# Kernel optimization log

Hardware: AMD Instinct MI355X
Metric: run time of the kernel (lower is better)

## Reference

```python
import jax, jax.numpy as jnp
import numpy as np

N, ND, NPAIR, KS = 131072, 32, 6, 3  # batch, dijetFeatures, 6 dijets, kernel=stride=3

def setup_inputs() -> dict:
    key = jax.random.key(0)
    k1, k2, k3, k4 = jax.random.split(key, 4)
    x = jax.random.normal(k1, (N, ND, 2 * NPAIR), dtype=jnp.float32)
    d = jax.random.normal(k2, (N, ND, NPAIR), dtype=jnp.float32)
    # Conv1d(nd, nd, 3, stride=3) params, torch layout [out_ch, in_ch, k]
    fan_in = ND * KS
    W = jax.random.normal(k3, (ND, ND, KS), dtype=jnp.float32) / np.float32(np.sqrt(fan_in))
    b = jax.random.normal(k4, (ND,), dtype=jnp.float32) * 0.01
    return {"x": x, "d": d, "W": W, "b": b}

def reference(x, d, W, b):
    n = x.shape[0]
    # reinforce interleave: (j0 j1 d0 | j2 j3 d1 | ...) -> [n, nd, 6, 3]
    # x[:, :, 2s:2s+2] followed by d[:, :, s] for each of the 6 slots.
    din = jnp.concatenate([x.reshape(n, ND, NPAIR, 2), d[..., None]], axis=3)
    # Conv1d kernel=stride=3 over the length-18 interleaved seq == per-slot contraction
    out = jnp.einsum('ncsk,ock->nos', din, W) + b[None, :, None]
    return out  # [n, nd, 6]
```

## Files before the change

### kernel.cpp

```cpp
#include <hip/hip_runtime.h>


#define ND 32
#define NPAIR 6
#define SPB 32
#define BT 192
#define COLS (SPB * NPAIR)
#define KSTR 104
#define OSTR 200

typedef __attribute__((ext_vector_type(8))) short bf16x8;
typedef __attribute__((ext_vector_type(4))) float f32x4;

__device__ __forceinline__ unsigned pack2(float lo, float hi) {
    return __builtin_amdgcn_perm(__float_as_uint(hi), __float_as_uint(lo), 0x07060302u);
}
__device__ __forceinline__ unsigned short bf16t(float v) {
    return (unsigned short)(__float_as_uint(v) >> 16);
}

__global__ __launch_bounds__(BT) void dijet_mfma(
    const float* __restrict__ x,
    const float* __restrict__ d,
    const float* __restrict__ W,
    const float* __restrict__ bias,
    float* __restrict__ out,
    int N)
{
    __shared__ __align__(16) unsigned char smem[COLS * KSTR * 2 + ND * KSTR * 2];
    unsigned short* Bb = (unsigned short*)smem;
    unsigned short* Ab = (unsigned short*)(smem + COLS * KSTR * 2);
    float* obuf = (float*)smem;

    const int t  = threadIdx.x;
    const int n0 = blockIdx.x * SPB;
    const bool full = (n0 + SPB <= N);

    const float* xb = x + (size_t)n0 * (ND * 2 * NPAIR);
#pragma unroll
    for (int i = 0; i < 16; ++i) {
        int fl = 4 * (t + i * BT);
        int ls = fl / 384;
        int r  = fl % 384;
        int c  = r / 12;
        int e  = r % 12;
        float4 v;
        if (full || n0 + ls < N) v = *(const float4*)(xb + fl);
        else v = make_float4(0.f, 0.f, 0.f, 0.f);
        int col0 = ls * NPAIR + (e >> 1);
        *(unsigned*)&Bb[col0 * KSTR + 2 * c]       = pack2(v.x, v.y);
        *(unsigned*)&Bb[(col0 + 1) * KSTR + 2 * c] = pack2(v.z, v.w);
    }

    const float* db = d + (size_t)n0 * (ND * NPAIR);
#pragma unroll
    for (int i = 0; i < 8; ++i) {
        int fl = 4 * (t + i * BT);
        float4 v;
        if (full) v = *(const float4*)(db + fl);
        else {
            float tmp[4];
#pragma unroll
            for (int m = 0; m < 4; ++m) {
                int f = fl + m;
                tmp[m] = (n0 + f / 192 < N) ? db[f] : 0.f;
            }
            v = make_float4(tmp[0], tmp[1], tmp[2], tmp[3]);
        }
        float vv[4] = {v.x, v.y, v.z, v.w};
#pragma unroll
        for (int m = 0; m < 4; ++m) {
            int f  = fl + m;
            int ls = f / 192;
            int r  = f % 192;
            int c  = r / 6;
            int s  = r % 6;
            Bb[(ls * NPAIR + s) * KSTR + 64 + c] = bf16t(vv[m]);
        }
    }

#pragma unroll
    for (int i = 0; i < 16; ++i) {
        int idx = t + i * BT;
        int o = idx / 96;
        int r = idx % 96;
        int c = r / 3;
        int j = r % 3;
        int k = (j == 2) ? (64 + c) : (2 * c + j);
        Ab[o * KSTR + k] = bf16t(W[idx]);
    }

    __syncthreads();

    const int w     = t >> 6;
    const int l     = t & 63;
    const int row16 = l & 15;
    const int quad  = l >> 4;
    const int ct0   = w * 4;

    bf16x8 Af[2][3];
#pragma unroll
    for (int ot = 0; ot < 2; ++ot) {
        const unsigned short* ap = Ab + (ot * 16 + row16) * KSTR + quad * 8;
#pragma unroll
        for (int ks = 0; ks < 3; ++ks)
            Af[ot][ks] = *(const bf16x8*)(ap + ks * 32);
    }

    float4 bv0 = *(const float4*)(bias + quad * 4);
    float4 bv1 = *(const float4*)(bias + 16 + quad * 4);
    f32x4 acc[4][2];
#pragma unroll
    for (int ct = 0; ct < 4; ++ct) {
        acc[ct][0] = (f32x4){bv0.x, bv0.y, bv0.z, bv0.w};
        acc[ct][1] = (f32x4){bv1.x, bv1.y, bv1.z, bv1.w};
    }

#pragma unroll
    for (int ct = 0; ct < 4; ++ct) {
        int col = (ct0 + ct) * 16 + row16;
        const unsigned short* bp = Bb + col * KSTR + quad * 8;
        bf16x8 B0 = *(const bf16x8*)(bp);
        bf16x8 B1 = *(const bf16x8*)(bp + 32);
        bf16x8 B2 = *(const bf16x8*)(bp + 64);
        acc[ct][0] = __builtin_amdgcn_mfma_f32_16x16x32_bf16(Af[0][0], B0, acc[ct][0], 0, 0, 0);
        acc[ct][0] = __builtin_amdgcn_mfma_f32_16x16x32_bf16(Af[0][1], B1, acc[ct][0], 0, 0, 0);
        acc[ct][0] = __builtin_amdgcn_mfma_f32_16x16x32_bf16(Af[0][2], B2, acc[ct][0], 0, 0, 0);
        acc[ct][1] = __builtin_amdgcn_mfma_f32_16x16x32_bf16(Af[1][0], B0, acc[ct][1], 0, 0, 0);
        acc[ct][1] = __builtin_amdgcn_mfma_f32_16x16x32_bf16(Af[1][1], B1, acc[ct][1], 0, 0, 0);
        acc[ct][1] = __builtin_amdgcn_mfma_f32_16x16x32_bf16(Af[1][2], B2, acc[ct][1], 0, 0, 0);
    }

    __syncthreads();

#pragma unroll
    for (int ct = 0; ct < 4; ++ct) {
        int col = (ct0 + ct) * 16 + row16;
        int ls  = col / 6;
        int s   = col % 6;
        float* ob = obuf + ls * OSTR + s;
#pragma unroll
        for (int ot = 0; ot < 2; ++ot) {
            int o0 = ot * 16 + quad * 4;
            ob[(o0 + 0) * NPAIR] = acc[ct][ot].x;
            ob[(o0 + 1) * NPAIR] = acc[ct][ot].y;
            ob[(o0 + 2) * NPAIR] = acc[ct][ot].z;
            ob[(o0 + 3) * NPAIR] = acc[ct][ot].w;
        }
    }

    __syncthreads();

    float* og = out + (size_t)n0 * (ND * NPAIR);
#pragma unroll
    for (int k = 0; k < 8; ++k) {
        int F  = 4 * (t + k * BT);
        int ns = F / 192;
        int wi = F % 192;
        if (full || n0 + ns < N) {
            float4 v = *(const float4*)(obuf + ns * OSTR + wi);
            *(float4*)(og + ns * 192 + wi) = v;
        }
    }
}

extern "C" void kernel_launch(void* const* d_in, const int* in_sizes, int n_in,
                              void* d_out, int out_size, void* d_ws, size_t ws_size,
                              hipStream_t stream) {
    const float* x = (const float*)d_in[0];
    const float* d = (const float*)d_in[1];
    const float* W = (const float*)d_in[2];
    const float* b = (const float*)d_in[3];
    float* out = (float*)d_out;

    int N = in_sizes[0] / (ND * 2 * NPAIR);
    int blocks = (N + SPB - 1) / SPB;

    dijet_mfma<<<blocks, BT, 0, stream>>>(x, d, W, b, out, N);
}
```

Measured before the change: 391.0 us.

## Load MFMA operands directly from global memory, dropping LDS staging

Removes the shared-memory staging of x, d and W as bf16. Each lane now gathers its MFMA B-fragment straight from global memory with float2 and scalar loads and packs to bf16 in registers. The A-fragments are built the same way from W. This drops a barrier and the LDS write/read traffic, and shrinks LDS use, which may allow higher occupancy. The cost is strided, less coalesced global loads (float2 at stride 12, scalars at stride 6) and redundant W reads per wave, which rely on cache hits.

After: 391.9 us. About the same (+0.3%).

```diff
diff --git a/kernel.cpp b/kernel.cpp
--- a/kernel.cpp
+++ b/kernel.cpp
@@ -5,18 +5,15 @@
 #define NPAIR 6
 #define SPB 32
 #define BT 192
-#define COLS (SPB * NPAIR)
-#define KSTR 104
 #define OSTR 200
 
 typedef __attribute__((ext_vector_type(8))) short bf16x8;
 typedef __attribute__((ext_vector_type(4))) float f32x4;
 
+union BU { unsigned u[4]; bf16x8 v; };
+
 __device__ __forceinline__ unsigned pack2(float lo, float hi) {
     return __builtin_amdgcn_perm(__float_as_uint(hi), __float_as_uint(lo), 0x07060302u);
-}
-__device__ __forceinline__ unsigned short bf16t(float v) {
-    return (unsigned short)(__float_as_uint(v) >> 16);
 }
 
 __global__ __launch_bounds__(BT) void dijet_mfma(
@@ -27,70 +24,11 @@
     float* __restrict__ out,
     int N)
 {
-    __shared__ __align__(16) unsigned char smem[COLS * KSTR * 2 + ND * KSTR * 2];
-    unsigned short* Bb = (unsigned short*)smem;
-    unsigned short* Ab = (unsigned short*)(smem + COLS * KSTR * 2);
-    float* obuf = (float*)smem;
+    __shared__ __align__(16) float obuf[SPB * OSTR];
 
-    const int t  = threadIdx.x;
-    const int n0 = blockIdx.x * SPB;
+    const int t    = threadIdx.x;
+    const int n0   = blockIdx.x * SPB;
     const bool full = (n0 + SPB <= N);
-
-    const float* xb = x + (size_t)n0 * (ND * 2 * NPAIR);
-#pragma unroll
-    for (int i = 0; i < 16; ++i) {
-        int fl = 4 * (t + i * BT);
-        int ls = fl / 384;
-        int r  = fl % 384;
-        int c  = r / 12;
-        int e  = r % 12;
-        float4 v;
-        if (full || n0 + ls < N) v = *(const float4*)(xb + fl);
-        else v = make_float4(0.f, 0.f, 0.f, 0.f);
-        int col0 = ls * NPAIR + (e >> 1);
-        *(unsigned*)&Bb[col0 * KSTR + 2 * c]       = pack2(v.x, v.y);
-        *(unsigned*)&Bb[(col0 + 1) * KSTR + 2 * c] = pack2(v.z, v.w);
-    }
-
-    const float* db = d + (size_t)n0 * (ND * NPAIR);
-#pragma unroll
-    for (int i = 0; i < 8; ++i) {
-        int fl = 4 * (t + i * BT);
-        float4 v;
-        if (full) v = *(const float4*)(db + fl);
-        else {
-            float tmp[4];
-#pragma unroll
-            for (int m = 0; m < 4; ++m) {
-                int f = fl + m;
-                tmp[m] = (n0 + f / 192 < N) ? db[f] : 0.f;
-            }
-            v = make_float4(tmp[0], tmp[1], tmp[2], tmp[3]);
-        }
-        float vv[4] = {v.x, v.y, v.z, v.w};
-#pragma unroll
-        for (int m = 0; m < 4; ++m) {
-            int f  = fl + m;
-            int ls = f / 192;
-            int r  = f % 192;
-            int c  = r / 6;
-            int s  = r % 6;
-            Bb[(ls * NPAIR + s) * KSTR + 64 + c] = bf16t(vv[m]);
-        }
-    }
-
-#pragma unroll
-    for (int i = 0; i < 16; ++i) {
-        int idx = t + i * BT;
-        int o = idx / 96;
-        int r = idx % 96;
-        int c = r / 3;
-        int j = r % 3;
-        int k = (j == 2) ? (64 + c) : (2 * c + j);
-        Ab[o * KSTR + k] = bf16t(W[idx]);
-    }
-
-    __syncthreads();
 
     const int w     = t >> 6;
     const int l     = t & 63;
@@ -101,10 +39,24 @@
     bf16x8 Af[2][3];
 #pragma unroll
     for (int ot = 0; ot < 2; ++ot) {
-        const unsigned short* ap = Ab + (ot * 16 + row16) * KSTR + quad * 8;
+        const float* wb = W + (ot * 16 + row16) * 96;
+        const float* wq = wb + quad * 12;
 #pragma unroll
-        for (int ks = 0; ks < 3; ++ks)
-            Af[ot][ks] = *(const bf16x8*)(ap + ks * 32);
+        for (int ks = 0; ks < 2; ++ks) {
+            BU b;
+#pragma unroll
+            for (int cc = 0; cc < 4; ++cc) {
+                const float* p = wq + (16 * ks + cc) * 3;
+                b.u[cc] = pack2(p[0], p[1]);
+            }
+            Af[ot][ks] = b.v;
+        }
+        const float* wq2 = wb + quad * 24 + 2;
+        BU b2;
+#pragma unroll
+        for (int m = 0; m < 4; ++m)
+            b2.u[m] = pack2(wq2[(2 * m) * 3], wq2[(2 * m + 1) * 3]);
+        Af[ot][2] = b2.v;
     }
 
     float4 bv0 = *(const float4*)(bias + quad * 4);
@@ -118,30 +70,52 @@
 
 #pragma unroll
     for (int ct = 0; ct < 4; ++ct) {
-        int col = (ct0 + ct) * 16 + row16;
-        const unsigned short* bp = Bb + col * KSTR + quad * 8;
-        bf16x8 B0 = *(const bf16x8*)(bp);
-        bf16x8 B1 = *(const bf16x8*)(bp + 32);
-        bf16x8 B2 = *(const bf16x8*)(bp + 64);
-        acc[ct][0] = __builtin_amdgcn_mfma_f32_16x16x32_bf16(Af[0][0], B0, acc[ct][0], 0, 0, 0);
-        acc[ct][0] = __builtin_amdgcn_mfma_f32_16x16x32_bf16(Af[0][1], B1, acc[ct][0], 0, 0, 0);
-        acc[ct][0] = __builtin_amdgcn_mfma_f32_16x16x32_bf16(Af[0][2], B2, acc[ct][0], 0, 0, 0);
-        acc[ct][1] = __builtin_amdgcn_mfma_f32_16x16x32_bf16(Af[1][0], B0, acc[ct][1], 0, 0, 0);
-        acc[ct][1] = __builtin_amdgcn_mfma_f32_16x16x32_bf16(Af[1][1], B1, acc[ct][1], 0, 0, 0);
-        acc[ct][1] = __builtin_amdgcn_mfma_f32_16x16x32_bf16(Af[1][2], B2, acc[ct][1], 0, 0, 0);
+        const int col = (ct0 + ct) * 16 + row16;
+        const int ls  = col / 6;
+        const int s   = col - ls * 6;
+        const bool ok = full || (n0 + ls < N);
+
+        const float* xp = x + (size_t)(n0 + ls) * 384 + quad * 48 + 2 * s;
+        const float* dp = d + (size_t)(n0 + ls) * 192 + quad * 48 + s;
+
+        float2 v0[4], v1[4];
+        float  vd[8];
+#pragma unroll
+        for (int cc = 0; cc < 4; ++cc) {
+            v0[cc] = ok ? *(const float2*)(xp + cc * 12)       : make_float2(0.f, 0.f);
+            v1[cc] = ok ? *(const float2*)(xp + 192 + cc * 12) : make_float2(0.f, 0.f);
+        }
+#pragma unroll
+        for (int j = 0; j < 8; ++j)
+            vd[j] = ok ? dp[j * 6] : 0.f;
+
+        BU b0, b1, b2;
+#pragma unroll
+        for (int cc = 0; cc < 4; ++cc) {
+            b0.u[cc] = pack2(v0[cc].x, v0[cc].y);
+            b1.u[cc] = pack2(v1[cc].x, v1[cc].y);
+        }
+#pragma unroll
+        for (int m = 0; m < 4; ++m)
+            b2.u[m] = pack2(vd[2 * m], vd[2 * m + 1]);
+
+        acc[ct][0] = __builtin_amdgcn_mfma_f32_16x16x32_bf16(Af[0][0], b0.v, acc[ct][0], 0, 0, 0);
+        acc[ct][0] = __builtin_amdgcn_mfma_f32_16x16x32_bf16(Af[0][1], b1.v, acc[ct][0], 0, 0, 0);
+        acc[ct][0] = __builtin_amdgcn_mfma_f32_16x16x32_bf16(Af[0][2], b2.v, acc[ct][0], 0, 0, 0);
+        acc[ct][1] = __builtin_amdgcn_mfma_f32_16x16x32_bf16(Af[1][0], b0.v, acc[ct][1], 0, 0, 0);
+        acc[ct][1] = __builtin_amdgcn_mfma_f32_16x16x32_bf16(Af[1][1], b1.v, acc[ct][1], 0, 0, 0);
+        acc[ct][1] = __builtin_amdgcn_mfma_f32_16x16x32_bf16(Af[1][2], b2.v, acc[ct][1], 0, 0, 0);
     }
-
-    __syncthreads();
 
 #pragma unroll
     for (int ct = 0; ct < 4; ++ct) {
-        int col = (ct0 + ct) * 16 + row16;
-        int ls  = col / 6;
-        int s   = col % 6;
+        const int col = (ct0 + ct) * 16 + row16;
+        const int ls  = col / 6;
+        const int s   = col - ls * 6;
         float* ob = obuf + ls * OSTR + s;
 #pragma unroll
         for (int ot = 0; ot < 2; ++ot) {
-            int o0 = ot * 16 + quad * 4;
+            const int o0 = ot * 16 + quad * 4;
             ob[(o0 + 0) * NPAIR] = acc[ct][ot].x;
             ob[(o0 + 1) * NPAIR] = acc[ct][ot].y;
             ob[(o0 + 2) * NPAIR] = acc[ct][ot].z;
@@ -154,9 +128,9 @@
     float* og = out + (size_t)n0 * (ND * NPAIR);
 #pragma unroll
     for (int k = 0; k < 8; ++k) {
-        int F  = 4 * (t + k * BT);
-        int ns = F / 192;
-        int wi = F % 192;
+        const int F  = 4 * (t + k * BT);
+        const int ns = F / 192;
+        const int wi = F % 192;
         if (full || n0 + ns < N) {
             float4 v = *(const float4*)(obuf + ns * OSTR + wi);
             *(float4*)(og + ns * 192 + wi) = v;
```
